# Kernel optimization log

Measured on AMD Instinct MI355X. Metric: run time of the kernel, lower is better.

Reference implementation:

```python
import jax, jax.numpy as jnp
import numpy as np

N_USERS = 100000
N_ITEMS = 150000
N_NODES = N_USERS + N_ITEMS
N_EDGES = 4000000
LATENT_DIM = 64
N_LAYERS = 3


def setup_inputs() -> dict:
    key = jax.random.key(0)
    k1, k2, k3, k4, k5 = jax.random.split(key, 5)
    user_emb = 0.1 * jax.random.normal(k1, (N_USERS, LATENT_DIM), dtype=jnp.float32)
    item_emb = 0.1 * jax.random.normal(k2, (N_ITEMS, LATENT_DIM), dtype=jnp.float32)
    # COO representation of the symmetric-normalized adjacency D^-1/2 A D^-1/2
    edge_src = jax.random.randint(k3, (N_EDGES,), 0, N_NODES, dtype=jnp.int32)
    edge_dst = jax.random.randint(k4, (N_EDGES,), 0, N_NODES, dtype=jnp.int32)
    edge_vals = jax.random.uniform(k5, (N_EDGES,), dtype=jnp.float32)
    return {"user_emb": user_emb, "item_emb": item_emb, "edge_vals": edge_vals,
            "edge_src": edge_src, "edge_dst": edge_dst}


def _spmm(edge_src, edge_dst, edge_vals, x):
    # y[dst] += val * x[src]  (equivalent of torch.sparse.mm(graph, x))
    msgs = edge_vals[:, None] * x[edge_src]  # [E, d]
    return jax.ops.segment_sum(msgs, edge_dst, num_segments=N_NODES)


def reference(user_emb, item_emb, edge_vals, edge_src, edge_dst):
    # LightGCN.computer(): n_layers of SpMM propagation + layer-stack mean pool
    all_emb = jnp.concatenate([user_emb, item_emb], axis=0)  # [N, d]
    acc = all_emb  # running sum over layer stack (layer 0)
    x = all_emb
    for _ in range(N_LAYERS):
        x = _spmm(edge_src, edge_dst, edge_vals, x)
        acc = acc + x
    light_out = acc / jnp.asarray(N_LAYERS + 1, dtype=acc.dtype)
    users = light_out[:N_USERS]
    items = light_out[N_USERS:]
    return users, items
```

## Files before the change

### kernel.cpp

```cpp
#include <hip/hip_runtime.h>
#include <hip/hip_bf16.h>

#define N_USERS 100000
#define N_ITEMS 150000
#define N_NODES 250000
#define N_EDGES 4000000
#define DIM     64
#define N_ELEM  (N_NODES * DIM)
#define U_ELEM  (N_USERS * DIM)
#define BSHIFT  10
#define BNODES  (1 << BSHIFT)
#define NBUCKET ((N_NODES + BNODES - 1) >> BSHIFT)
#define CHUNK   4096
#define NB_HIST ((N_EDGES + CHUNK - 1) / CHUNK)

typedef _Float16 h2 __attribute__((ext_vector_type(2)));

__device__ __forceinline__ float bflo(unsigned int u) { return __uint_as_float(u << 16); }
__device__ __forceinline__ float bfhi(unsigned int u) { return __uint_as_float(u & 0xffff0000u); }
__device__ __forceinline__ unsigned int bfr(float f) {
    unsigned int u = __float_as_uint(f);
    return (u + 0x7fffu + ((u >> 16) & 1u)) >> 16;
}
__device__ __forceinline__ unsigned int pk(float a, float b) {
    return bfr(a) | (bfr(b) << 16);
}
__device__ __forceinline__ h2 uh(unsigned int u) {
    union { unsigned int u; h2 h; } c; c.u = u; return c.h;
}
__device__ __forceinline__ unsigned int pkh(float a, float b) {
    union { h2 h; unsigned int u; } c;
    c.h.x = (_Float16)a; c.h.y = (_Float16)b;
    return c.u;
}

__global__ void probe_dtype(const unsigned short* __restrict__ ue, int* __restrict__ flag,
                            int* __restrict__ tot) {
    int lane = threadIdx.x;
    for (int b = lane; b < NBUCKET; b += 64) tot[b] = 0;
    int bad = 0;
    #pragma unroll
    for (int k = 0; k < 8; ++k) {
        unsigned int b = ((unsigned int)ue[lane * 8 + k]) << 16;
        float f = fabsf(__uint_as_float(b));
        if (!(f < 1.0f)) bad = 1;
    }
    unsigned long long m = __ballot(bad);
    if (lane == 0) flag[0] = (m == 0ULL) ? 1 : 0;
}

__global__ void hist_bucket(const int* __restrict__ dst, int* __restrict__ M,
                            int* __restrict__ tot) {
    __shared__ int h[NBUCKET];
    for (int b = threadIdx.x; b < NBUCKET; b += blockDim.x) h[b] = 0;
    __syncthreads();
    int base = blockIdx.x * CHUNK;
    int n = N_EDGES - base; if (n > CHUNK) n = CHUNK;
    for (int i = threadIdx.x; i < n; i += blockDim.x)
        atomicAdd(&h[dst[base + i] >> BSHIFT], 1);
    __syncthreads();
    for (int b = threadIdx.x; b < NBUCKET; b += blockDim.x) {
        int c = h[b];
        M[blockIdx.x * NBUCKET + b] = c;
        if (c) atomicAdd(&tot[b], c);
    }
}

__global__ void scan_bbase(const int* __restrict__ tot, int* __restrict__ bbase,
                           int* __restrict__ gres, int* __restrict__ row_ptr) {
    __shared__ int sh[256];
    int b = threadIdx.x;
    int v = (b < NBUCKET) ? tot[b] : 0;
    sh[b] = v;
    __syncthreads();
    for (int off = 1; off < 256; off <<= 1) {
        int t = (b >= off) ? sh[b - off] : 0;
        __syncthreads();
        sh[b] += t;
        __syncthreads();
    }
    if (b < NBUCKET) {
        int ex = sh[b] - v;
        bbase[b] = ex;
        gres[b]  = ex;
    }
    if (b == 0) { bbase[NBUCKET] = N_EDGES; row_ptr[N_NODES] = N_EDGES; }
}

__global__ void bin_scatter(const int* __restrict__ src, const int* __restrict__ dst,
                            const void* __restrict__ valsv, const int* __restrict__ flag,
                            const int* __restrict__ M, int* __restrict__ gres,
                            int2* __restrict__ aux) {
    __shared__ int  gb[NBUCKET];
    __shared__ int  lcur[NBUCKET];
    __shared__ int  sc[256];
    __shared__ int2 stage[CHUNK];
    __shared__ unsigned short sb[CHUNK];
    int tid = threadIdx.x;
    int base = blockIdx.x * CHUNK;
    int n = N_EDGES - base; if (n > CHUNK) n = CHUNK;

    int v = (tid < NBUCKET) ? M[blockIdx.x * NBUCKET + tid] : 0;
    sc[tid] = v;
    __syncthreads();
    for (int off = 1; off < 256; off <<= 1) {
        int t = (tid >= off) ? sc[tid - off] : 0;
        __syncthreads();
        sc[tid] += t;
        __syncthreads();
    }
    if (tid < NBUCKET) {
        int lb = sc[tid] - v;
        lcur[tid] = lb;
        gb[tid] = v ? (atomicAdd(&gres[tid], v) - lb) : 0;
    }
    __syncthreads();

    const int isbf = *flag;
    for (int i = tid; i < n; i += 256) {
        int e = base + i;
        int d = dst[e];
        int b = d >> BSHIFT;
        int pos = atomicAdd(&lcur[b], 1);
        float vv = isbf ? __bfloat162float(((const __hip_bfloat16*)valsv)[e])
                        : ((const float*)valsv)[e];
        int2 r;
        r.x = src[e] | ((d & (BNODES - 1)) << 18);
        r.y = __float_as_int(vv);
        stage[pos] = r;
        sb[pos] = (unsigned short)b;
    }
    __syncthreads();
    for (int j = tid; j < n; j += 256) {
        int b = sb[j];
        aux[gb[b] + j] = stage[j];
    }
}

__global__ void bucket_csr(const int* __restrict__ bbase, const int2* __restrict__ aux,
                           int* __restrict__ row_ptr, int2* __restrict__ sedge) {
    __shared__ int h[BNODES];
    __shared__ int c[BNODES];
    int b  = blockIdx.x;
    int n0 = b << BSHIFT;
    int nd = N_NODES - n0; if (nd > BNODES) nd = BNODES;
    int lo = bbase[b], hi = bbase[b + 1];
    int t = threadIdx.x;
    h[t] = 0;
    __syncthreads();
    for (int e = lo + t; e < hi; e += blockDim.x)
        atomicAdd(&h[(aux[e].x >> 18) & (BNODES - 1)], 1);
    __syncthreads();
    int v = h[t];
    c[t] = v;
    __syncthreads();
    for (int off = 1; off < BNODES; off <<= 1) {
        int u = (t >= off) ? c[t - off] : 0;
        __syncthreads();
        c[t] += u;
        __syncthreads();
    }
    int gbase = lo + c[t] - v;
    if (t < nd) row_ptr[n0 + t] = gbase;
    c[t] = gbase;
    __syncthreads();
    for (int e = lo + t; e < hi; e += blockDim.x) {
        int2 r = aux[e];
        int pos = atomicAdd(&c[(r.x >> 18) & (BNODES - 1)], 1);
        int2 o; o.x = r.x & 0x3FFFF; o.y = r.y;
        sedge[pos] = o;
    }
}

__global__ void init_kernel(const void* __restrict__ uev, const void* __restrict__ iev,
                            const int* __restrict__ flag,
                            unsigned int* __restrict__ x,
                            void* __restrict__ outacc) {
    int i4 = blockIdx.x * blockDim.x + threadIdx.x;
    if (i4 >= N_ELEM / 4) return;
    const int isbf = *flag;
    float v0, v1, v2, v3;
    if (i4 < U_ELEM / 4) {
        if (isbf) {
            uint2 u = ((const uint2*)uev)[i4];
            v0 = bflo(u.x); v1 = bfhi(u.x); v2 = bflo(u.y); v3 = bfhi(u.y);
        } else {
            float4 f = ((const float4*)uev)[i4];
            v0 = f.x; v1 = f.y; v2 = f.z; v3 = f.w;
        }
    } else {
        int j4 = i4 - U_ELEM / 4;
        if (isbf) {
            uint2 u = ((const uint2*)iev)[j4];
            v0 = bflo(u.x); v1 = bfhi(u.x); v2 = bflo(u.y); v3 = bfhi(u.y);
        } else {
            float4 f = ((const float4*)iev)[j4];
            v0 = f.x; v1 = f.y; v2 = f.z; v3 = f.w;
        }
    }
    uint2 pv; pv.x = pkh(v0, v1); pv.y = pkh(v2, v3);
    ((uint2*)x)[i4] = pv;
    if (outacc) {
        if (isbf) {
            uint2 o; o.x = pk(0.25f * v0, 0.25f * v1); o.y = pk(0.25f * v2, 0.25f * v3);
            ((uint2*)outacc)[i4] = o;
        } else {
            float4 f; f.x = 0.25f * v0; f.y = 0.25f * v1; f.z = 0.25f * v2; f.w = 0.25f * v3;
            ((float4*)outacc)[i4] = f;
        }
    }
}

template <int MODE>
__global__ void spmm_csr(const int* __restrict__ row_ptr,
                         const int2* __restrict__ sedge,
                         const unsigned int* __restrict__ x,
                         unsigned int* __restrict__ xn,
                         const unsigned int* __restrict__ p0,
                         const unsigned int* __restrict__ p1,
                         void* __restrict__ outv,
                         const int* __restrict__ flag) {
    int lane = threadIdx.x & 63;
    int g = lane >> 3;
    int q16 = (lane & 7) << 4;
    int w = (blockIdx.x * blockDim.x + threadIdx.x) >> 6;
    if (w >= N_NODES) return;
    const int isbf = *flag;
    int beg = row_ptr[w], end = row_ptr[w + 1];

    const char* xb = (const char*)x;
    float s0 = 0.f, s1 = 0.f, s2 = 0.f, s3 = 0.f, s4 = 0.f, s5 = 0.f, s6 = 0.f, s7 = 0.f;
    float t0 = 0.f, t1 = 0.f, t2 = 0.f, t3 = 0.f, t4 = 0.f, t5 = 0.f, t6 = 0.f, t7 = 0.f;

    if (beg < end) {
        int em1 = end - 1;
        int e0 = beg + g, e1 = beg + 8 + g, e2 = beg + 16 + g, e3 = beg + 24 + g;
        int2 r0 = sedge[e0 <= em1 ? e0 : em1];
        int2 r1 = sedge[e1 <= em1 ? e1 : em1];
        int2 r2 = sedge[e2 <= em1 ? e2 : em1];
        int2 r3 = sedge[e3 <= em1 ? e3 : em1];
        uint4 v0 = *(const uint4*)(xb + ((r0.x << 7) + q16));
        uint4 v1 = *(const uint4*)(xb + ((r1.x << 7) + q16));
        uint4 v2 = *(const uint4*)(xb + ((r2.x << 7) + q16));
        uint4 v3 = *(const uint4*)(xb + ((r3.x << 7) + q16));
        float w0 = (e0 <= em1) ? __int_as_float(r0.y) : 0.f;
        float w1 = (e1 <= em1) ? __int_as_float(r1.y) : 0.f;
        float w2 = (e2 <= em1) ? __int_as_float(r2.y) : 0.f;
        float w3 = (e3 <= em1) ? __int_as_float(r3.y) : 0.f;
        {
            h2 a0 = uh(v0.x), a1 = uh(v0.y), a2 = uh(v0.z), a3 = uh(v0.w);
            s0 = fmaf((float)a0.x, w0, s0); s1 = fmaf((float)a0.y, w0, s1);
            s2 = fmaf((float)a1.x, w0, s2); s3 = fmaf((float)a1.y, w0, s3);
            s4 = fmaf((float)a2.x, w0, s4); s5 = fmaf((float)a2.y, w0, s5);
            s6 = fmaf((float)a3.x, w0, s6); s7 = fmaf((float)a3.y, w0, s7);
        }
        {
            h2 a0 = uh(v1.x), a1 = uh(v1.y), a2 = uh(v1.z), a3 = uh(v1.w);
            t0 = fmaf((float)a0.x, w1, t0); t1 = fmaf((float)a0.y, w1, t1);
            t2 = fmaf((float)a1.x, w1, t2); t3 = fmaf((float)a1.y, w1, t3);
            t4 = fmaf((float)a2.x, w1, t4); t5 = fmaf((float)a2.y, w1, t5);
            t6 = fmaf((float)a3.x, w1, t6); t7 = fmaf((float)a3.y, w1, t7);
        }
        {
            h2 a0 = uh(v2.x), a1 = uh(v2.y), a2 = uh(v2.z), a3 = uh(v2.w);
            s0 = fmaf((float)a0.x, w2, s0); s1 = fmaf((float)a0.y, w2, s1);
            s2 = fmaf((float)a1.x, w2, s2); s3 = fmaf((float)a1.y, w2, s3);
            s4 = fmaf((float)a2.x, w2, s4); s5 = fmaf((float)a2.y, w2, s5);
            s6 = fmaf((float)a3.x, w2, s6); s7 = fmaf((float)a3.y, w2, s7);
        }
        {
            h2 a0 = uh(v3.x), a1 = uh(v3.y), a2 = uh(v3.z), a3 = uh(v3.w);
            t0 = fmaf((float)a0.x, w3, t0); t1 = fmaf((float)a0.y, w3, t1);
            t2 = fmaf((float)a1.x, w3, t2); t3 = fmaf((float)a1.y, w3, t3);
            t4 = fmaf((float)a2.x, w3, t4); t5 = fmaf((float)a2.y, w3, t5);
            t6 = fmaf((float)a3.x, w3, t6); t7 = fmaf((float)a3.y, w3, t7);
        }
        for (int eb16 = beg + 32; eb16 < end; eb16 += 16) {
            int ea = eb16 + g, eb = eb16 + 8 + g;
            int2 ra = sedge[ea <= em1 ? ea : em1];
            int2 rb = sedge[eb <= em1 ? eb : em1];
            uint4 va = *(const uint4*)(xb + ((ra.x << 7) + q16));
            uint4 vb = *(const uint4*)(xb + ((rb.x << 7) + q16));
            float wa = (ea <= em1) ? __int_as_float(ra.y) : 0.f;
            float wb = (eb <= em1) ? __int_as_float(rb.y) : 0.f;
            h2 a0 = uh(va.x), a1 = uh(va.y), a2 = uh(va.z), a3 = uh(va.w);
            h2 b0 = uh(vb.x), b1 = uh(vb.y), b2 = uh(vb.z), b3 = uh(vb.w);
            s0 = fmaf((float)a0.x, wa, s0); s1 = fmaf((float)a0.y, wa, s1);
            s2 = fmaf((float)a1.x, wa, s2); s3 = fmaf((float)a1.y, wa, s3);
            s4 = fmaf((float)a2.x, wa, s4); s5 = fmaf((float)a2.y, wa, s5);
            s6 = fmaf((float)a3.x, wa, s6); s7 = fmaf((float)a3.y, wa, s7);
            t0 = fmaf((float)b0.x, wb, t0); t1 = fmaf((float)b0.y, wb, t1);
            t2 = fmaf((float)b1.x, wb, t2); t3 = fmaf((float)b1.y, wb, t3);
            t4 = fmaf((float)b2.x, wb, t4); t5 = fmaf((float)b2.y, wb, t5);
            t6 = fmaf((float)b3.x, wb, t6); t7 = fmaf((float)b3.y, wb, t7);
        }
    }
    s0 += t0; s1 += t1; s2 += t2; s3 += t3;
    s4 += t4; s5 += t5; s6 += t6; s7 += t7;

    s0 += __shfl_xor(s0, 8);  s1 += __shfl_xor(s1, 8);
    s2 += __shfl_xor(s2, 8);  s3 += __shfl_xor(s3, 8);
    s4 += __shfl_xor(s4, 8);  s5 += __shfl_xor(s5, 8);
    s6 += __shfl_xor(s6, 8);  s7 += __shfl_xor(s7, 8);
    s0 += __shfl_xor(s0, 16); s1 += __shfl_xor(s1, 16);
    s2 += __shfl_xor(s2, 16); s3 += __shfl_xor(s3, 16);
    s4 += __shfl_xor(s4, 16); s5 += __shfl_xor(s5, 16);
    s6 += __shfl_xor(s6, 16); s7 += __shfl_xor(s7, 16);
    s0 += __shfl_xor(s0, 32); s1 += __shfl_xor(s1, 32);
    s2 += __shfl_xor(s2, 32); s3 += __shfl_xor(s3, 32);
    s4 += __shfl_xor(s4, 32); s5 += __shfl_xor(s5, 32);
    s6 += __shfl_xor(s6, 32); s7 += __shfl_xor(s7, 32);

    if (g != 0) return;
    size_t oq = (size_t)w * 8 + (lane & 7);

    if (MODE == 0) {
        uint4 pv;
        pv.x = pkh(s0, s1); pv.y = pkh(s2, s3); pv.z = pkh(s4, s5); pv.w = pkh(s6, s7);
        ((uint4*)xn)[oq] = pv;
    } else if (MODE == 1) {
        uint4 a = ((const uint4*)p0)[oq];
        uint4 b = ((const uint4*)p1)[oq];
        uint4 c = ((const uint4*)x)[oq];
        h2 A0 = uh(a.x), A1 = uh(a.y), A2 = uh(a.z), A3 = uh(a.w);
        h2 B0 = uh(b.x), B1 = uh(b.y), B2 = uh(b.z), B3 = uh(b.w);
        h2 C0 = uh(c.x), C1 = uh(c.y), C2 = uh(c.z), C3 = uh(c.w);
        float r0 = 0.25f * (s0 + (float)A0.x + (float)B0.x + (float)C0.x);
        float r1 = 0.25f * (s1 + (float)A0.y + (float)B0.y + (float)C0.y);
        float r2 = 0.25f * (s2 + (float)A1.x + (float)B1.x + (float)C1.x);
        float r3 = 0.25f * (s3 + (float)A1.y + (float)B1.y + (float)C1.y);
        float r4 = 0.25f * (s4 + (float)A2.x + (float)B2.x + (float)C2.x);
        float r5 = 0.25f * (s5 + (float)A2.y + (float)B2.y + (float)C2.y);
        float r6 = 0.25f * (s6 + (float)A3.x + (float)B3.x + (float)C3.x);
        float r7 = 0.25f * (s7 + (float)A3.y + (float)B3.y + (float)C3.y);
        if (isbf) {
            uint4 pv;
            pv.x = pk(r0, r1); pv.y = pk(r2, r3); pv.z = pk(r4, r5); pv.w = pk(r6, r7);
            ((uint4*)outv)[oq] = pv;
        } else {
            float4 f0; f0.x = r0; f0.y = r1; f0.z = r2; f0.w = r3;
            float4 f1; f1.x = r4; f1.y = r5; f1.z = r6; f1.w = r7;
            ((float4*)outv)[2 * oq]     = f0;
            ((float4*)outv)[2 * oq + 1] = f1;
        }
    } else if (MODE == 2) {
        uint4 pv;
        pv.x = pkh(s0, s1); pv.y = pkh(s2, s3); pv.z = pkh(s4, s5); pv.w = pkh(s6, s7);
        ((uint4*)xn)[oq] = pv;
        if (isbf) {
            uint4 ov = ((uint4*)outv)[oq];
            float r0 = bflo(ov.x) + 0.25f * s0;
            float r1 = bfhi(ov.x) + 0.25f * s1;
            float r2 = bflo(ov.y) + 0.25f * s2;
            float r3 = bfhi(ov.y) + 0.25f * s3;
            float r4 = bflo(ov.z) + 0.25f * s4;
            float r5 = bfhi(ov.z) + 0.25f * s5;
            float r6 = bflo(ov.w) + 0.25f * s6;
            float r7 = bfhi(ov.w) + 0.25f * s7;
            uint4 nv;
            nv.x = pk(r0, r1); nv.y = pk(r2, r3); nv.z = pk(r4, r5); nv.w = pk(r6, r7);
            ((uint4*)outv)[oq] = nv;
        } else {
            float4 o0 = ((float4*)outv)[2 * oq];
            float4 o1 = ((float4*)outv)[2 * oq + 1];
            o0.x += 0.25f * s0; o0.y += 0.25f * s1; o0.z += 0.25f * s2; o0.w += 0.25f * s3;
            o1.x += 0.25f * s4; o1.y += 0.25f * s5; o1.z += 0.25f * s6; o1.w += 0.25f * s7;
            ((float4*)outv)[2 * oq]     = o0;
            ((float4*)outv)[2 * oq + 1] = o1;
        }
    } else {
        if (isbf) {
            uint4 ov = ((uint4*)outv)[oq];
            float r0 = bflo(ov.x) + 0.25f * s0;
            float r1 = bfhi(ov.x) + 0.25f * s1;
            float r2 = bflo(ov.y) + 0.25f * s2;
            float r3 = bfhi(ov.y) + 0.25f * s3;
            float r4 = bflo(ov.z) + 0.25f * s4;
            float r5 = bfhi(ov.z) + 0.25f * s5;
            float r6 = bflo(ov.w) + 0.25f * s6;
            float r7 = bfhi(ov.w) + 0.25f * s7;
            uint4 nv;
            nv.x = pk(r0, r1); nv.y = pk(r2, r3); nv.z = pk(r4, r5); nv.w = pk(r6, r7);
            ((uint4*)outv)[oq] = nv;
        } else {
            float4 o0 = ((float4*)outv)[2 * oq];
            float4 o1 = ((float4*)outv)[2 * oq + 1];
            o0.x += 0.25f * s0; o0.y += 0.25f * s1; o0.z += 0.25f * s2; o0.w += 0.25f * s3;
            o1.x += 0.25f * s4; o1.y += 0.25f * s5; o1.z += 0.25f * s6; o1.w += 0.25f * s7;
            ((float4*)outv)[2 * oq]     = o0;
            ((float4*)outv)[2 * oq + 1] = o1;
        }
    }
}

static inline size_t align256(size_t x) { return (x + 255) & ~(size_t)255; }

extern "C" void kernel_launch(void* const* d_in, const int* in_sizes, int n_in,
                              void* d_out, int out_size, void* d_ws, size_t ws_size,
                              hipStream_t stream) {
    const int* es = (const int*)d_in[3];
    const int* ed = (const int*)d_in[4];

    char* wsb = (char*)d_ws;
    size_t off = 0;
    int*  flag    = (int*)wsb;               off = align256(off + sizeof(int));
    int*  tot     = (int*)(wsb + off);       off = align256(off + (size_t)NBUCKET * 4);
    int*  bbase   = (int*)(wsb + off);       off = align256(off + (size_t)(NBUCKET + 1) * 4);
    int*  gres    = (int*)(wsb + off);       off = align256(off + (size_t)NBUCKET * 4);
    int*  M       = (int*)(wsb + off);       off = align256(off + (size_t)NB_HIST * NBUCKET * 4);
    int*  row_ptr = (int*)(wsb + off);       off = align256(off + (size_t)(N_NODES + 1) * 4);
    int2* sedge   = (int2*)(wsb + off);      off = align256(off + (size_t)N_EDGES * 8);
    size_t z_off = off;
    int2* aux = (int2*)(wsb + z_off);

    const size_t hbuf = (size_t)N_ELEM * 2;

    const int eb = 256;
    const int egrid = (N_ELEM / 4 + eb - 1) / eb;
    const int sgrid = (N_NODES + 3) / 4;

    probe_dtype<<<1, 64, 0, stream>>>((const unsigned short*)d_in[0], flag, tot);
    hist_bucket<<<NB_HIST, eb, 0, stream>>>(ed, M, tot);
    scan_bbase<<<1, 256, 0, stream>>>(tot, bbase, gres, row_ptr);
    bin_scatter<<<NB_HIST, eb, 0, stream>>>(es, ed, d_in[2], flag, M, gres, aux);
    bucket_csr<<<NBUCKET, BNODES, 0, stream>>>(bbase, aux, row_ptr, sedge);

    size_t need_t1 = z_off + 3 * hbuf;

    if (ws_size >= need_t1) {
        unsigned int* x0 = (unsigned int*)(wsb + z_off);
        unsigned int* x1 = (unsigned int*)(wsb + z_off + hbuf);
        unsigned int* x2 = (unsigned int*)(wsb + z_off + 2 * hbuf);
        init_kernel<<<egrid, eb, 0, stream>>>(d_in[0], d_in[1], flag, x0, nullptr);
        spmm_csr<0><<<sgrid, eb, 0, stream>>>(row_ptr, sedge, x0, x1, nullptr, nullptr, nullptr, flag);
        spmm_csr<0><<<sgrid, eb, 0, stream>>>(row_ptr, sedge, x1, x2, nullptr, nullptr, nullptr, flag);
        spmm_csr<1><<<sgrid, eb, 0, stream>>>(row_ptr, sedge, x2, nullptr, x0, x1, d_out, flag);
    } else {
        unsigned int* x  = (unsigned int*)(wsb + z_off);
        unsigned int* xn = (unsigned int*)(wsb + z_off + hbuf);
        init_kernel<<<egrid, eb, 0, stream>>>(d_in[0], d_in[1], flag, x, d_out);
        spmm_csr<2><<<sgrid, eb, 0, stream>>>(row_ptr, sedge, x,  xn, nullptr, nullptr, d_out, flag);
        spmm_csr<2><<<sgrid, eb, 0, stream>>>(row_ptr, sedge, xn, x,  nullptr, nullptr, d_out, flag);
        spmm_csr<3><<<sgrid, eb, 0, stream>>>(row_ptr, sedge, x,  nullptr, nullptr, nullptr, d_out, flag);
    }
}
```

Measured before the change: 546.6 us.

## Vectorize preprocessing loads, fold dtype probe into histogram, add nontemporal memory ops

The separate probe kernel is merged into the first block of hist_bucket, and the bucket-total zeroing moves to hipMemsetAsync. The histogram, scatter and bucket-CSR loops now read edges with int4 vector loads. The SpMM kernels use nontemporal loads and stores for the edge stream and for the output and previous-layer buffers, aiming to keep the gathered embedding rows resident in cache. This trades a kernel launch for a memset and risks slower streaming if the nontemporal hints interact badly with the cache.

```diff
diff --git a/kernel.cpp b/kernel.cpp
--- a/kernel.cpp
+++ b/kernel.cpp
@@ -15,6 +15,8 @@
 #define NB_HIST ((N_EDGES + CHUNK - 1) / CHUNK)
 
 typedef _Float16 h2 __attribute__((ext_vector_type(2)));
+typedef unsigned int u32x4 __attribute__((ext_vector_type(4)));
+typedef float f32x4 __attribute__((ext_vector_type(4)));
 
 __device__ __forceinline__ float bflo(unsigned int u) { return __uint_as_float(u << 16); }
 __device__ __forceinline__ float bfhi(unsigned int u) { return __uint_as_float(u & 0xffff0000u); }
@@ -33,30 +35,57 @@
     c.h.x = (_Float16)a; c.h.y = (_Float16)b;
     return c.u;
 }
-
-__global__ void probe_dtype(const unsigned short* __restrict__ ue, int* __restrict__ flag,
-                            int* __restrict__ tot) {
-    int lane = threadIdx.x;
-    for (int b = lane; b < NBUCKET; b += 64) tot[b] = 0;
-    int bad = 0;
-    #pragma unroll
-    for (int k = 0; k < 8; ++k) {
-        unsigned int b = ((unsigned int)ue[lane * 8 + k]) << 16;
-        float f = fabsf(__uint_as_float(b));
-        if (!(f < 1.0f)) bad = 1;
-    }
-    unsigned long long m = __ballot(bad);
-    if (lane == 0) flag[0] = (m == 0ULL) ? 1 : 0;
-}
-
-__global__ void hist_bucket(const int* __restrict__ dst, int* __restrict__ M,
+__device__ __forceinline__ int2 ldnt2(const int2* p) {
+    unsigned long long u = __builtin_nontemporal_load((const unsigned long long*)p);
+    int2 r; r.x = (int)u; r.y = (int)(u >> 32); return r;
+}
+__device__ __forceinline__ uint4 ldnt4(const void* p) {
+    u32x4 v = __builtin_nontemporal_load((const u32x4*)p);
+    uint4 r; r.x = v.x; r.y = v.y; r.z = v.z; r.w = v.w; return r;
+}
+__device__ __forceinline__ void stnt4(void* p, uint4 v) {
+    u32x4 t; t.x = v.x; t.y = v.y; t.z = v.z; t.w = v.w;
+    __builtin_nontemporal_store(t, (u32x4*)p);
+}
+__device__ __forceinline__ void stnt4f(void* p, float4 v) {
+    f32x4 t; t.x = v.x; t.y = v.y; t.z = v.z; t.w = v.w;
+    __builtin_nontemporal_store(t, (f32x4*)p);
+}
+__device__ __forceinline__ float4 ldnt4f(const void* p) {
+    f32x4 v = __builtin_nontemporal_load((const f32x4*)p);
+    float4 r; r.x = v.x; r.y = v.y; r.z = v.z; r.w = v.w; return r;
+}
+
+__global__ void hist_bucket(const int* __restrict__ dst, const unsigned short* __restrict__ ue,
+                            int* __restrict__ flag, int* __restrict__ M,
                             int* __restrict__ tot) {
     __shared__ int h[NBUCKET];
     for (int b = threadIdx.x; b < NBUCKET; b += blockDim.x) h[b] = 0;
+    if (blockIdx.x == 0 && threadIdx.x < 64) {
+        int lane = threadIdx.x;
+        int bad = 0;
+        #pragma unroll
+        for (int k = 0; k < 8; ++k) {
+            unsigned int b = ((unsigned int)ue[lane * 8 + k]) << 16;
+            float f = fabsf(__uint_as_float(b));
+            if (!(f < 1.0f)) bad = 1;
+        }
+        unsigned long long m = __ballot(bad);
+        if (lane == 0) flag[0] = (m == 0ULL) ? 1 : 0;
+    }
     __syncthreads();
     int base = blockIdx.x * CHUNK;
     int n = N_EDGES - base; if (n > CHUNK) n = CHUNK;
-    for (int i = threadIdx.x; i < n; i += blockDim.x)
+    const int4* d4p = (const int4*)(dst + base);
+    int n4 = n >> 2;
+    for (int i = threadIdx.x; i < n4; i += blockDim.x) {
+        int4 d = d4p[i];
+        atomicAdd(&h[d.x >> BSHIFT], 1);
+        atomicAdd(&h[d.y >> BSHIFT], 1);
+        atomicAdd(&h[d.z >> BSHIFT], 1);
+        atomicAdd(&h[d.w >> BSHIFT], 1);
+    }
+    for (int i = (n4 << 2) + (int)threadIdx.x; i < n; i += blockDim.x)
         atomicAdd(&h[dst[base + i] >> BSHIFT], 1);
     __syncthreads();
     for (int b = threadIdx.x; b < NBUCKET; b += blockDim.x) {
@@ -117,7 +146,36 @@
     __syncthreads();
 
     const int isbf = *flag;
-    for (int i = tid; i < n; i += 256) {
+    const int4* d4p = (const int4*)(dst + base);
+    const int4* s4p = (const int4*)(src + base);
+    int n4 = n >> 2;
+    for (int i = tid; i < n4; i += 256) {
+        int4 d = d4p[i];
+        int4 s = s4p[i];
+        float v0, v1, v2, v3;
+        if (isbf) {
+            uint2 u = ((const uint2*)valsv)[(base >> 2) + i];
+            v0 = bflo(u.x); v1 = bfhi(u.x); v2 = bflo(u.y); v3 = bfhi(u.y);
+        } else {
+            float4 f = ((const float4*)valsv)[(base >> 2) + i];
+            v0 = f.x; v1 = f.y; v2 = f.z; v3 = f.w;
+        }
+        int b0 = d.x >> BSHIFT, b1 = d.y >> BSHIFT, b2 = d.z >> BSHIFT, b3 = d.w >> BSHIFT;
+        int p0 = atomicAdd(&lcur[b0], 1);
+        int p1 = atomicAdd(&lcur[b1], 1);
+        int p2 = atomicAdd(&lcur[b2], 1);
+        int p3 = atomicAdd(&lcur[b3], 1);
+        int2 r;
+        r.x = s.x | ((d.x & (BNODES - 1)) << 18); r.y = __float_as_int(v0);
+        stage[p0] = r; sb[p0] = (unsigned short)b0;
+        r.x = s.y | ((d.y & (BNODES - 1)) << 18); r.y = __float_as_int(v1);
+        stage[p1] = r; sb[p1] = (unsigned short)b1;
+        r.x = s.z | ((d.z & (BNODES - 1)) << 18); r.y = __float_as_int(v2);
+        stage[p2] = r; sb[p2] = (unsigned short)b2;
+        r.x = s.w | ((d.w & (BNODES - 1)) << 18); r.y = __float_as_int(v3);
+        stage[p3] = r; sb[p3] = (unsigned short)b3;
+    }
+    for (int i = (n4 << 2) + tid; i < n; i += 256) {
         int e = base + i;
         int d = dst[e];
         int b = d >> BSHIFT;
@@ -148,8 +206,21 @@
     int t = threadIdx.x;
     h[t] = 0;
     __syncthreads();
-    for (int e = lo + t; e < hi; e += blockDim.x)
-        atomicAdd(&h[(aux[e].x >> 18) & (BNODES - 1)], 1);
+    if (hi > lo) {
+        int lo2 = (lo + 1) & ~1;
+        if (t == 0 && lo < lo2)
+            atomicAdd(&h[(aux[lo].x >> 18) & (BNODES - 1)], 1);
+        int np = (hi - lo2) >> 1;
+        const int4* ap = (const int4*)aux;
+        for (int i = t; i < np; i += BNODES) {
+            int4 two = ap[(lo2 >> 1) + i];
+            atomicAdd(&h[(two.x >> 18) & (BNODES - 1)], 1);
+            atomicAdd(&h[(two.z >> 18) & (BNODES - 1)], 1);
+        }
+        int rem = lo2 + (np << 1);
+        if (t == 0 && rem < hi)
+            atomicAdd(&h[(aux[rem].x >> 18) & (BNODES - 1)], 1);
+    }
     __syncthreads();
     int v = h[t];
     c[t] = v;
@@ -235,10 +306,10 @@
     if (beg < end) {
         int em1 = end - 1;
         int e0 = beg + g, e1 = beg + 8 + g, e2 = beg + 16 + g, e3 = beg + 24 + g;
-        int2 r0 = sedge[e0 <= em1 ? e0 : em1];
-        int2 r1 = sedge[e1 <= em1 ? e1 : em1];
-        int2 r2 = sedge[e2 <= em1 ? e2 : em1];
-        int2 r3 = sedge[e3 <= em1 ? e3 : em1];
+        int2 r0 = ldnt2(&sedge[e0 <= em1 ? e0 : em1]);
+        int2 r1 = ldnt2(&sedge[e1 <= em1 ? e1 : em1]);
+        int2 r2 = ldnt2(&sedge[e2 <= em1 ? e2 : em1]);
+        int2 r3 = ldnt2(&sedge[e3 <= em1 ? e3 : em1]);
         uint4 v0 = *(const uint4*)(xb + ((r0.x << 7) + q16));
         uint4 v1 = *(const uint4*)(xb + ((r1.x << 7) + q16));
         uint4 v2 = *(const uint4*)(xb + ((r2.x << 7) + q16));
@@ -277,8 +348,8 @@
         }
         for (int eb16 = beg + 32; eb16 < end; eb16 += 16) {
             int ea = eb16 + g, eb = eb16 + 8 + g;
-            int2 ra = sedge[ea <= em1 ? ea : em1];
-            int2 rb = sedge[eb <= em1 ? eb : em1];
+            int2 ra = ldnt2(&sedge[ea <= em1 ? ea : em1]);
+            int2 rb = ldnt2(&sedge[eb <= em1 ? eb : em1]);
             uint4 va = *(const uint4*)(xb + ((ra.x << 7) + q16));
             uint4 vb = *(const uint4*)(xb + ((rb.x << 7) + q16));
             float wa = (ea <= em1) ? __int_as_float(ra.y) : 0.f;
@@ -317,10 +388,10 @@
     if (MODE == 0) {
         uint4 pv;
         pv.x = pkh(s0, s1); pv.y = pkh(s2, s3); pv.z = pkh(s4, s5); pv.w = pkh(s6, s7);
-        ((uint4*)xn)[oq] = pv;
+        stnt4(&((uint4*)xn)[oq], pv);
     } else if (MODE == 1) {
-        uint4 a = ((const uint4*)p0)[oq];
-        uint4 b = ((const uint4*)p1)[oq];
+        uint4 a = ldnt4(&((const uint4*)p0)[oq]);
+        uint4 b = ldnt4(&((const uint4*)p1)[oq]);
         uint4 c = ((const uint4*)x)[oq];
         h2 A0 = uh(a.x), A1 = uh(a.y), A2 = uh(a.z), A3 = uh(a.w);
         h2 B0 = uh(b.x), B1 = uh(b.y), B2 = uh(b.z), B3 = uh(b.w);
@@ -336,19 +407,19 @@
         if (isbf) {
             uint4 pv;
             pv.x = pk(r0, r1); pv.y = pk(r2, r3); pv.z = pk(r4, r5); pv.w = pk(r6, r7);
-            ((uint4*)outv)[oq] = pv;
+            stnt4(&((uint4*)outv)[oq], pv);
         } else {
             float4 f0; f0.x = r0; f0.y = r1; f0.z = r2; f0.w = r3;
             float4 f1; f1.x = r4; f1.y = r5; f1.z = r6; f1.w = r7;
-            ((float4*)outv)[2 * oq]     = f0;
-            ((float4*)outv)[2 * oq + 1] = f1;
+            stnt4f(&((float4*)outv)[2 * oq], f0);
+            stnt4f(&((float4*)outv)[2 * oq + 1], f1);
         }
     } else if (MODE == 2) {
         uint4 pv;
         pv.x = pkh(s0, s1); pv.y = pkh(s2, s3); pv.z = pkh(s4, s5); pv.w = pkh(s6, s7);
-        ((uint4*)xn)[oq] = pv;
-        if (isbf) {
-            uint4 ov = ((uint4*)outv)[oq];
+        stnt4(&((uint4*)xn)[oq], pv);
+        if (isbf) {
+            uint4 ov = ldnt4(&((uint4*)outv)[oq]);
             float r0 = bflo(ov.x) + 0.25f * s0;
             float r1 = bfhi(ov.x) + 0.25f * s1;
             float r2 = bflo(ov.y) + 0.25f * s2;
@@ -359,18 +430,18 @@
             float r7 = bfhi(ov.w) + 0.25f * s7;
             uint4 nv;
             nv.x = pk(r0, r1); nv.y = pk(r2, r3); nv.z = pk(r4, r5); nv.w = pk(r6, r7);
-            ((uint4*)outv)[oq] = nv;
-        } else {
-            float4 o0 = ((float4*)outv)[2 * oq];
-            float4 o1 = ((float4*)outv)[2 * oq + 1];
+            stnt4(&((uint4*)outv)[oq], nv);
+        } else {
+            float4 o0 = ldnt4f(&((float4*)outv)[2 * oq]);
+            float4 o1 = ldnt4f(&((float4*)outv)[2 * oq + 1]);
             o0.x += 0.25f * s0; o0.y += 0.25f * s1; o0.z += 0.25f * s2; o0.w += 0.25f * s3;
             o1.x += 0.25f * s4; o1.y += 0.25f * s5; o1.z += 0.25f * s6; o1.w += 0.25f * s7;
-            ((float4*)outv)[2 * oq]     = o0;
-            ((float4*)outv)[2 * oq + 1] = o1;
+            stnt4f(&((float4*)outv)[2 * oq], o0);
+            stnt4f(&((float4*)outv)[2 * oq + 1], o1);
         }
     } else {
         if (isbf) {
-            uint4 ov = ((uint4*)outv)[oq];
+            uint4 ov = ldnt4(&((uint4*)outv)[oq]);
             float r0 = bflo(ov.x) + 0.25f * s0;
             float r1 = bfhi(ov.x) + 0.25f * s1;
             float r2 = bflo(ov.y) + 0.25f * s2;
@@ -381,14 +452,14 @@
             float r7 = bfhi(ov.w) + 0.25f * s7;
             uint4 nv;
             nv.x = pk(r0, r1); nv.y = pk(r2, r3); nv.z = pk(r4, r5); nv.w = pk(r6, r7);
-            ((uint4*)outv)[oq] = nv;
-        } else {
-            float4 o0 = ((float4*)outv)[2 * oq];
-            float4 o1 = ((float4*)outv)[2 * oq + 1];
+            stnt4(&((uint4*)outv)[oq], nv);
+        } else {
+            float4 o0 = ldnt4f(&((float4*)outv)[2 * oq]);
+            float4 o1 = ldnt4f(&((float4*)outv)[2 * oq + 1]);
             o0.x += 0.25f * s0; o0.y += 0.25f * s1; o0.z += 0.25f * s2; o0.w += 0.25f * s3;
             o1.x += 0.25f * s4; o1.y += 0.25f * s5; o1.z += 0.25f * s6; o1.w += 0.25f * s7;
-            ((float4*)outv)[2 * oq]     = o0;
-            ((float4*)outv)[2 * oq + 1] = o1;
+            stnt4f(&((float4*)outv)[2 * oq], o0);
+            stnt4f(&((float4*)outv)[2 * oq + 1], o1);
         }
     }
 }
@@ -419,8 +490,8 @@
     const int egrid = (N_ELEM / 4 + eb - 1) / eb;
     const int sgrid = (N_NODES + 3) / 4;
 
-    probe_dtype<<<1, 64, 0, stream>>>((const unsigned short*)d_in[0], flag, tot);
-    hist_bucket<<<NB_HIST, eb, 0, stream>>>(ed, M, tot);
+    hipMemsetAsync(tot, 0, (size_t)NBUCKET * 4, stream);
+    hist_bucket<<<NB_HIST, eb, 0, stream>>>(ed, (const unsigned short*)d_in[0], flag, M, tot);
     scan_bbase<<<1, 256, 0, stream>>>(tot, bbase, gres, row_ptr);
     bin_scatter<<<NB_HIST, eb, 0, stream>>>(es, ed, d_in[2], flag, M, gres, aux);
     bucket_csr<<<NBUCKET, BNODES, 0, stream>>>(bbase, aux, row_ptr, sedge);
```

New measurement: 559.3 us. 1.02x slower.
